# Performance work log

Measured on AMD Instinct MI355X. Metric: run time of the kernel, lower is better.

The kernel has to match this reference:

```python
import math
import jax, jax.numpy as jnp
import numpy as np

# dims (match init_kwargs)
B, NMHC, T, D = 4, 4, 1024, 256
DK, DATTN, H, E = 16, 512, 8, 4
DV = DATTN // H          # 64
DKP = 2 * DK             # 32 (PoPE doubles d_key)
HE = H * E
R = max(DK // 4, 1)      # 4
DA = int(DK * 1.618)     # 25
DPG = max(int(DATTN * 0.618), 1)  # 316
ND = NMHC * D
EPS = 1e-6
ROUTE_TEMP = 1.0

def _rms(x):
    return x * jax.lax.rsqrt(jnp.mean(x * x, axis=-1, keepdims=True) + EPS)

def _sinkhorn(M, n_iters=6):
    M = jnp.exp(M)
    for _ in range(n_iters):
        M = M / jnp.sum(M, axis=-1, keepdims=True)
        M = M / jnp.sum(M, axis=-2, keepdims=True)
    return M

def _l2norm(x):
    return x / jnp.maximum(jnp.linalg.norm(x, axis=-1, keepdims=True), 1e-12)

def _pope(x, phi):
    mu = jax.nn.softplus(x)
    return jnp.concatenate([mu * jnp.cos(phi), mu * jnp.sin(phi)], axis=-1)

def setup_inputs() -> dict:
    key = jax.random.key(0)
    ks = iter(jax.random.split(key, 40))
    rn = lambda shape, s=0.02: jax.random.normal(next(ks), shape, jnp.float32) * s
    return {
        'stream': jax.random.normal(next(ks), (B, NMHC, T, D), jnp.float32),
        'Wq': rn((H, D, DK)), 'Wk': rn((H, D, DK)), 'Wv': rn((H, D, DV)),
        'pope_delta': rn((DK,), 0.1),
        'q_router': rn((H, D, E), 0.05), 'kv_router': rn((H, D, E), 0.05),
        'lora_A_q': rn((HE, D, R), 0.01), 'lora_B_q': rn((HE, R, DK)),
        'lora_A_k': rn((HE, D, R), 0.01), 'lora_B_k': rn((HE, R, DK)),
        'lora_A_v': rn((HE, D, R), 0.01), 'lora_B_v': rn((HE, R, DV)),
        'alpha_up': rn((HE, D, DA), 0.01), 'alpha_down': rn((HE, DA, DKP), 0.01),
        'beta_up': rn((HE, D, DA), 0.01), 'beta_down': rn((HE, DA, 1), 0.01),
        'mhc_norm_w': jnp.ones((HE, ND)),
        'phi_pre': rn((HE, ND, NMHC)), 'phi_post': rn((HE, ND, NMHC)),
        'phi_res': rn((HE, ND, NMHC * NMHC)),
        'b_pre': jnp.zeros((HE, NMHC)), 'b_post': jnp.zeros((HE, NMHC)),
        'b_res': jnp.zeros((HE, NMHC, NMHC)),
        'a_pre': jnp.ones((HE,)), 'a_post': jnp.ones((HE,)), 'a_res': jnp.ones((HE,)),
        'norm_w': jnp.ones((HE, D)),
        'W_pre': rn((HE, D, DATTN), 0.01),
        'W_o': rn((DATTN, D)),
        'W_pg1': rn((HE, D, DPG), 0.01), 'W_pg2': rn((HE, DPG, D), 0.01),
    }

def _forward(stream, Wq, Wk, Wv, pope_delta, q_router, kv_router,
             lora_A_q, lora_B_q, lora_A_k, lora_B_k, lora_A_v, lora_B_v,
             alpha_up, alpha_down, beta_up, beta_down,
             mhc_norm_w, phi_pre, phi_post, phi_res, b_pre, b_post, b_res,
             a_pre, a_post, a_res, norm_w, W_pre, W_o, W_pg1, W_pg2):
    dt = stream.dtype
    freqs = 10000.0 ** (jnp.arange(DK, dtype=dt) / DK)
    pos = jnp.arange(T, dtype=dt)
    phi_q = pos[:, None] * freqs[None, :]                       # (T,DK)
    phi_k = phi_q - 2.0 * math.pi * jax.nn.sigmoid(pope_delta)  # key phase shift

    # MHC RMSNorm has no bias; fold its per-expert weight into the phi matrices
    x_hat = _rms(jnp.reshape(jnp.swapaxes(stream, 1, 2), (B, T, ND)))
    route_in = jnp.mean(stream, axis=1)                         # (B,T,D)

    q_logits = jnp.clip(jnp.einsum('btd,hde->hbte', route_in, q_router), -10, 10)
    q_probs = jax.nn.softmax(q_logits / ROUTE_TEMP, axis=-1)
    q_sel = jnp.argmax(q_logits, axis=-1)                       # (H,B,T) eval-mode routing
    kv_logits = jnp.clip(jnp.einsum('btd,hde->hbte', route_in, kv_router), -10, 10)
    kv_probs = jax.nn.softmax(kv_logits / ROUTE_TEMP, axis=-1)
    kv_sel = jnp.argmax(kv_logits, axis=-1)
    eidx = jnp.arange(E)

    acc_pre = jnp.zeros((B, T, H * DV), dt)
    acc_post = jnp.zeros((B, T, D), dt)
    acc_res = jnp.zeros((B, T, NMHC, NMHC), dt)
    acc_hpost = jnp.zeros((B, T, NMHC), dt)
    outs = []
    for h in range(H):
        s = slice(h * E, (h + 1) * E)
        nw = mhc_norm_w[s][:, :, None]
        Hpre = jax.nn.sigmoid(a_pre[s][:, None, None, None] * jnp.einsum('btk,ekn->ebtn', x_hat, nw * phi_pre[s]) + b_pre[s][:, None, None, :])
        Hpost = 2.0 * jax.nn.sigmoid(a_post[s][:, None, None, None] * jnp.einsum('btk,ekn->ebtn', x_hat, nw * phi_post[s]) + b_post[s][:, None, None, :])
        res_l = jnp.einsum('btk,ekm->ebtm', x_hat, nw * phi_res[s]).reshape(E, B, T, NMHC, NMHC)
        Hres = _sinkhorn(a_res[s][:, None, None, None, None] * res_l + b_res[s][:, None, None, :, :])

        he = jnp.einsum('ebtn,bntd->ebtd', Hpre, stream)        # (E,B,T,D)
        he = _rms(he) * norm_w[s][:, None, None, :]

        # straight-through routing weights (forward == hard mask)
        qp = jnp.moveaxis(q_probs[h], -1, 0)[..., None]         # (E,B,T,1)
        qm = (q_sel[h][None] == eidx[:, None, None]).astype(dt)[..., None]
        eff_q = qp + jax.lax.stop_gradient(qm - qp)
        kp = jnp.moveaxis(kv_probs[h], -1, 0)[..., None]
        km = (kv_sel[h][None] == eidx[:, None, None]).astype(dt)[..., None]
        eff_kv = kp + jax.lax.stop_gradient(km - kp)

        # Q path (expert 0 is a no-op for Q)
        dq = jnp.einsum('ebtr,erk->ebtk', jax.nn.silu(jnp.einsum('ebtd,edr->ebtr', he, lora_A_q[s])), lora_B_q[s])
        q_e = _pope(_l2norm(jnp.einsum('ebtd,dk->ebtk', he, Wq[h]) + dq), phi_q)
        pg = jax.nn.sigmoid(jnp.einsum('ebtp,epd->ebtd', jax.nn.silu(jnp.einsum('ebtd,edp->ebtp', he, W_pg1[s])), W_pg2[s]))
        q_h = jnp.sum(eff_q[1:] * q_e[1:], axis=0)
        acc_post = acc_post + jnp.sum(eff_q[1:] * pg[1:], axis=0) / H

        # KV path (all experts)
        dk_ = jnp.einsum('ebtr,erk->ebtk', jax.nn.silu(jnp.einsum('ebtd,edr->ebtr', he, lora_A_k[s])), lora_B_k[s])
        k_e = _pope(_l2norm(jnp.einsum('ebtd,dk->ebtk', he, Wk[h]) + dk_), phi_k)
        dv_ = jnp.einsum('ebtr,erk->ebtk', jax.nn.silu(jnp.einsum('ebtd,edr->ebtr', he, lora_A_v[s])), lora_B_v[s])
        v_e = jax.nn.silu(jnp.einsum('ebtd,dk->ebtk', he, Wv[h]) + dv_)
        al_e = jax.nn.sigmoid(jnp.einsum('ebta,eak->ebtk', jax.nn.silu(jnp.einsum('ebtd,eda->ebta', he, alpha_up[s])), alpha_down[s]))
        be_e = jax.nn.sigmoid(jnp.einsum('ebta,eak->ebtk', jax.nn.silu(jnp.einsum('ebtd,eda->ebta', he, beta_up[s])), beta_down[s]))
        preg = jax.nn.silu(jnp.einsum('ebtd,edc->ebtc', he, W_pre[s]))
        k_h = jnp.sum(eff_kv * k_e, axis=0)
        v_h = jnp.sum(eff_kv * v_e, axis=0)
        al_h = jnp.sum(eff_kv * al_e, axis=0)
        be_h = jnp.sum(eff_kv * be_e, axis=0)
        acc_pre = acc_pre + jnp.sum(eff_kv * preg, axis=0) / H
        acc_res = acc_res + jnp.sum(Hres * eff_kv[..., None], axis=0)
        acc_hpost = acc_hpost + jnp.sum(Hpost * eff_kv, axis=0)

        # KDA delta-rule recurrence over T (state S: (B,DKP,DV))
        def step(S, inp):
            q_t, k_t, v_t, a_t, b_t = inp
            aS = a_t[:, :, None] * S
            kaS = jnp.einsum('bd,bde->be', k_t, aS)
            S_new = aS + b_t[:, :, None] * (k_t[:, :, None] * (v_t - kaS)[:, None, :])
            return S_new, jnp.einsum('bd,bde->be', q_t, S_new)
        xs = tuple(jnp.swapaxes(a, 0, 1) for a in (q_h, k_h, v_h, al_h, be_h))
        _, o = jax.lax.scan(step, jnp.zeros((B, DKP, DV), dt), xs)
        out_h = jnp.where((q_sel[h] == 0)[..., None], jnp.zeros((), dt), jnp.swapaxes(o, 0, 1))
        outs.append(out_h)

    concat = jnp.concatenate(outs, axis=-1) / math.sqrt(H * DV)
    result = (concat * acc_pre) @ W_o * acc_post                # (B,T,D)
    res = jnp.einsum('btij,bjtd->bitd', acc_res / H, stream)    # stream mixing
    return res + jnp.einsum('btn,btd->bntd', acc_hpost / H, result)

def reference(stream, Wq, Wk, Wv, pope_delta, q_router, kv_router,
              lora_A_q, lora_B_q, lora_A_k, lora_B_k, lora_A_v, lora_B_v,
              alpha_up, alpha_down, beta_up, beta_down,
              mhc_norm_w, phi_pre, phi_post, phi_res, b_pre, b_post, b_res,
              a_pre, a_post, a_res, norm_w, W_pre, W_o, W_pg1, W_pg2):
    return _forward(stream, Wq, Wk, Wv, pope_delta, q_router, kv_router,
                    lora_A_q, lora_B_q, lora_A_k, lora_B_k, lora_A_v, lora_B_v,
                    alpha_up, alpha_down, beta_up, beta_down,
                    mhc_norm_w, phi_pre, phi_post, phi_res, b_pre, b_post, b_res,
                    a_pre, a_post, a_res, norm_w, W_pre, W_o, W_pg1, W_pg2)
```

## Files before the change

### kernel.cpp

```cpp
#include <hip/hip_runtime.h>
#include <math.h>

#define B_ 4
#define NM 4
#define T_ 1024
#define D_ 256
#define DK_ 16
#define DV_ 64
#define DKP_ 32
#define H_ 8
#define E_ 4
#define HE_ 32
#define R_ 4
#define DA_ 25
#define DPG_ 316
#define ND_ 1024
#define DATTN_ 512
#define BT_ 4096
#define TB 16
#define TT 64

#define OFF_CNT     0
#define OFF_ACCPRE  256
#define OFF_ACCPOST (OFF_ACCPRE + BT_*512)
#define OFF_ACCRES  (OFF_ACCPOST + BT_*256)
#define OFF_ACCHP   (OFF_ACCRES + BT_*16)
#define OFF_QH      (OFF_ACCHP + BT_*4)
#define ZERO_END    (OFF_QH + H_*BT_*32)
#define OFF_KH      ZERO_END
#define OFF_VH      (OFF_KH + H_*BT_*32)
#define OFF_ALH     (OFF_VH + H_*BT_*64)
#define OFF_BEH     (OFF_ALH + H_*BT_*32)
#define OFF_LKV     (OFF_BEH + H_*BT_)
#define OFF_LQ      (OFF_LKV + HE_*BT_)
#define OFF_RMS     (OFF_LQ + HE_*BT_)
#define OFF_ATTN    (OFF_RMS + BT_)
#define OFF_TRIG    (OFF_ATTN + BT_*512)
#define WS_FLOATS   (OFF_TRIG + 4*T_*DK_)

__device__ __forceinline__ float sigf(float x){ return 1.0f/(1.0f+expf(-x)); }
__device__ __forceinline__ float siluf(float x){ return x/(1.0f+expf(-x)); }
__device__ __forceinline__ float softplusf(float x){ return fmaxf(x,0.0f)+log1pf(expf(-fabsf(x))); }

__global__ __launch_bounds__(256) void k_trig(const float* __restrict__ delta, float* __restrict__ ws){
  int idx = blockIdx.x*256 + threadIdx.x;
  int t = idx >> 4, k = idx & 15;
  double fr = pow(10000.0, (double)k / 16.0);
  float freq = (float)fr;
  float pq = (float)t * freq;
  float sg = sigf(delta[k]);
  float shift = (float)(2.0*M_PI) * sg;
  float pk = pq - shift;
  float* tr = ws + OFF_TRIG;
  tr[idx]         = (float)cos((double)pq);
  tr[16384+idx]   = (float)sin((double)pq);
  tr[32768+idx]   = (float)cos((double)pk);
  tr[49152+idx]   = (float)sin((double)pk);
}

__global__ __launch_bounds__(256) void k_route(const float* __restrict__ stream,
    const float* __restrict__ q_router, const float* __restrict__ kv_router,
    float* __restrict__ ws){
  __shared__ float s_route[256];
  __shared__ float s_red[4];
  __shared__ float s_log[64];
  int tok = blockIdx.x; int b = tok >> 10, t = tok & 1023;
  int d = threadIdx.x;
  const float* sp = stream + ((size_t)(b*4)*1024 + t)*256 + d;
  float s0 = sp[0];
  float s1 = sp[1024*256];
  float s2 = sp[2*1024*256];
  float s3 = sp[3*1024*256];
  s_route[d] = (((s0+s1)+s2)+s3)*0.25f;
  float ssp = s0*s0+s1*s1+s2*s2+s3*s3;
  for (int off=32; off; off>>=1) ssp += __shfl_xor(ssp, off, 64);
  if ((d & 63)==0) s_red[d>>6] = ssp;
  __syncthreads();
  if (d==0){
    float ss = ((s_red[0]+s_red[1])+s_red[2])+s_red[3];
    float mean = ss*(1.0f/1024.0f) + 1e-6f;
    ws[OFF_RMS + tok] = (float)(1.0/sqrt((double)mean));
  }
  if (d < 64){
    int lane = d;
    int r = lane>>5, h = (lane>>2)&7, e = lane&3;
    const float* R = (r ? kv_router : q_router) + h*1024 + e;
    float acc = 0.f;
    for (int dd=0; dd<256; ++dd) acc = fmaf(s_route[dd], R[dd*4], acc);
    s_log[lane] = fminf(fmaxf(acc,-10.f),10.f);
  }
  if (d < 16){
    int r = d>>3, h = d&7;
    int base = r*32 + h*4;
    int best=0; float bv = s_log[base];
    for (int e=1;e<4;e++){ float v=s_log[base+e]; if (v>bv){bv=v;best=e;} }
    int* cnt = (int*)ws;
    if (r==1){
      int* lst = (int*)(ws + OFF_LKV);
      int pos = atomicAdd(&cnt[h*4+best],1);
      lst[(h*4+best)*BT_ + pos] = tok;
    } else if (best>0){
      int* lst = (int*)(ws + OFF_LQ);
      int pos = atomicAdd(&cnt[32 + h*4+best],1);
      lst[(h*4+best)*BT_ + pos] = tok;
    }
  }
}

__global__ __launch_bounds__(256) void k_expert_kv(
    const float* __restrict__ stream, float* ws,
    const float* __restrict__ Wk, const float* __restrict__ Wv,
    const float* __restrict__ lora_A_k, const float* __restrict__ lora_B_k,
    const float* __restrict__ lora_A_v, const float* __restrict__ lora_B_v,
    const float* __restrict__ alpha_up, const float* __restrict__ alpha_down,
    const float* __restrict__ beta_up, const float* __restrict__ beta_down,
    const float* __restrict__ mhc_norm_w, const float* __restrict__ phi_pre,
    const float* __restrict__ phi_post, const float* __restrict__ phi_res,
    const float* __restrict__ b_pre, const float* __restrict__ b_post, const float* __restrict__ b_res,
    const float* __restrict__ a_pre, const float* __restrict__ a_post, const float* __restrict__ a_res,
    const float* __restrict__ norm_w, const float* __restrict__ W_pre)
{
  int g = blockIdx.y; int h = g>>2;
  const int* cnt = (const int*)ws;
  int c = cnt[g];
  int start = blockIdx.x*TB;
  if (start >= c) return;
  int nact = min(TB, c-start);

  __shared__ float s_he[TB][258];
  __shared__ float s_phi[24][128];
  __shared__ float s_dots[TB][24];
  __shared__ float s_nw[1024];
  __shared__ float s_gnw[256];
  __shared__ float s_lrk[TB][4];
  __shared__ float s_lrv[TB][4];
  __shared__ float s_au[TB][25];
  __shared__ float s_bu[TB][25];
  __shared__ int s_tok[TB];
  int tid = threadIdx.x;
  if (tid < TB) s_tok[tid] = (tid < nact) ? ((const int*)(ws + OFF_LKV))[g*BT_ + start + tid] : -1;
  for (int i=tid;i<1024;i+=256) s_nw[i] = mhc_norm_w[g*1024+i];
  s_gnw[tid] = norm_w[g*256+tid];
  __syncthreads();

  float aP = a_pre[g], aQ = a_post[g], aR = a_res[g];
  int hw = tid>>5, lane = tid&31;
  int ti0 = hw, ti1 = hw+8;
  int tok0 = s_tok[ti0], tok1 = s_tok[ti1];
  const float* sb0 = stream + (tok0>=0 ? ((size_t)(tok0>>10)*4*262144 + (size_t)(tok0&1023)*256) : 0);
  const float* sb1 = stream + (tok1>=0 ? ((size_t)(tok1>>10)*4*262144 + (size_t)(tok1&1023)*256) : 0);
  float rn0 = (tok0>=0) ? ws[OFF_RMS + tok0] : 0.f;
  float rn1 = (tok1>=0) ? ws[OFF_RMS + tok1] : 0.f;

  float dA0[24], dA1[24];
  #pragma unroll
  for (int n=0;n<24;++n){ dA0[n]=0.f; dA1[n]=0.f; }
  for (int cc=0; cc<8; ++cc){
    __syncthreads();
    {
      int kk = tid & 127;
      int np = tid >> 7;
      int kg = cc*128 + kk;
      #pragma unroll
      for (int it=0; it<12; ++it){
        int n = np + it*2;
        float v;
        if (n < 4)       v = phi_pre [(size_t)g*4096  + (size_t)kg*4  + n];
        else if (n < 8)  v = phi_post[(size_t)g*4096  + (size_t)kg*4  + (n-4)];
        else             v = phi_res [(size_t)g*16384 + (size_t)kg*16 + (n-8)];
        s_phi[n][kk] = v;
      }
    }
    __syncthreads();
    int rr = cc>>1;
    int off = (cc&1)*128 + lane*4;
    float4 x0 = *(const float4*)(sb0 + (size_t)rr*262144 + off);
    float4 x1 = *(const float4*)(sb1 + (size_t)rr*262144 + off);
    float4 nw4 = *(const float4*)(&s_nw[cc*128 + lane*4]);
    x0.x *= rn0*nw4.x; x0.y *= rn0*nw4.y; x0.z *= rn0*nw4.z; x0.w *= rn0*nw4.w;
    x1.x *= rn1*nw4.x; x1.y *= rn1*nw4.y; x1.z *= rn1*nw4.z; x1.w *= rn1*nw4.w;
    #pragma unroll
    for (int n=0;n<24;++n){
      float4 p4 = *(const float4*)(&s_phi[n][lane*4]);
      dA0[n] = fmaf(x0.w,p4.w,fmaf(x0.z,p4.z,fmaf(x0.y,p4.y,fmaf(x0.x,p4.x,dA0[n]))));
      dA1[n] = fmaf(x1.w,p4.w,fmaf(x1.z,p4.z,fmaf(x1.y,p4.y,fmaf(x1.x,p4.x,dA1[n]))));
    }
  }
  #pragma unroll
  for (int n=0;n<24;++n){
    float v0=dA0[n], v1=dA1[n];
    v0 += __shfl_xor(v0,16,32); v0 += __shfl_xor(v0,8,32); v0 += __shfl_xor(v0,4,32); v0 += __shfl_xor(v0,2,32); v0 += __shfl_xor(v0,1,32);
    v1 += __shfl_xor(v1,16,32); v1 += __shfl_xor(v1,8,32); v1 += __shfl_xor(v1,4,32); v1 += __shfl_xor(v1,2,32); v1 += __shfl_xor(v1,1,32);
    dA0[n]=v0; dA1[n]=v1;
  }
  float bp0=b_pre[g*4+0], bp1=b_pre[g*4+1], bp2=b_pre[g*4+2], bp3=b_pre[g*4+3];

  auto finish = [&](int ti, int tok, const float (&dAx)[24], const float* sbx){
    if (tok < 0){
      #pragma unroll
      for (int m=0;m<8;++m) s_he[ti][m*32+lane] = 0.f;
      return;
    }
    if (lane==0){
      #pragma unroll
      for (int n=0;n<24;++n) s_dots[ti][n] = dAx[n];
    }
    float g0 = sigf(aP*dAx[0]+bp0);
    float g1 = sigf(aP*dAx[1]+bp1);
    float g2 = sigf(aP*dAx[2]+bp2);
    float g3 = sigf(aP*dAx[3]+bp3);
    if (lane>=16 && lane<20){
      int n = lane-16;
      float hp = 2.f*sigf(aQ*s_dots[ti][4+n] + b_post[g*4+n]);
      unsafeAtomicAdd(ws + OFF_ACCHP + tok*4 + n, hp);
    }
    if (lane<16){
      float m = expf(aR*s_dots[ti][8+lane] + b_res[g*16+lane]);
      for (int itr=0; itr<6; ++itr){
        float rsum = m;
        rsum += __shfl_xor(rsum, 1, 4);
        rsum += __shfl_xor(rsum, 2, 4);
        m = m / rsum;
        float csum = m;
        csum += __shfl_xor(csum, 4, 16);
        csum += __shfl_xor(csum, 8, 16);
        m = m / csum;
      }
      unsafeAtomicAdd(ws + OFF_ACCRES + tok*16 + lane, m);
    }
    float he[8]; float ssp = 0.f;
    #pragma unroll
    for (int m=0;m<8;++m){
      int d = m*32+lane;
      float hv = fmaf(g3, sbx[3*262144+d], fmaf(g2, sbx[2*262144+d], fmaf(g1, sbx[262144+d], g0*sbx[d])));
      he[m]=hv; ssp = fmaf(hv,hv,ssp);
    }
    ssp += __shfl_xor(ssp,16,32); ssp += __shfl_xor(ssp,8,32); ssp += __shfl_xor(ssp,4,32);
    ssp += __shfl_xor(ssp,2,32);  ssp += __shfl_xor(ssp,1,32);
    float scale = (float)(1.0/sqrt((double)(ssp*(1.0f/256.0f)+1e-6f)));
    #pragma unroll
    for (int m=0;m<8;++m){
      int d = m*32+lane;
      s_he[ti][d] = he[m]*scale*s_gnw[d];
    }
  };
  finish(ti0, tok0, dA0, sb0);
  finish(ti1, tok1, dA1, sb1);
  __syncthreads();

  if (tid < 128){
    int tt = (tid & 63) >> 2, r = tid & 3;
    const float* A = (tid < 64 ? lora_A_k : lora_A_v) + g*1024 + r;
    float acc = 0.f;
    for (int dd=0; dd<256; ++dd) acc = fmaf(s_he[tt][dd], A[dd*4], acc);
    float sv = siluf(acc);
    if (tid<64) s_lrk[tt][r] = sv; else s_lrv[tt][r] = sv;
  }
  __syncthreads();
  {
    int tt = tid>>4, kk = tid&15;
    float acc=0.f;
    const float* Wkp = Wk + h*4096 + kk;
    for (int dd=0; dd<256; ++dd) acc = fmaf(s_he[tt][dd], Wkp[dd*16], acc);
    float dkv = 0.f;
    for (int r=0;r<4;r++) dkv = fmaf(s_lrk[tt][r], lora_B_k[g*64 + r*16 + kk], dkv);
    acc += dkv;
    float ssq = acc*acc;
    ssq += __shfl_xor(ssq, 1, 16);
    ssq += __shfl_xor(ssq, 2, 16);
    ssq += __shfl_xor(ssq, 4, 16);
    ssq += __shfl_xor(ssq, 8, 16);
    float den = fmaxf(sqrtf(ssq), 1e-12f);
    float xn = acc/den;
    float mu = softplusf(xn);
    if (tt < nact){
      int tok = s_tok[tt]; int t = tok&1023;
      float* kh = ws + OFF_KH + ((size_t)h*BT_ + tok)*32;
      const float* ck = ws + OFF_TRIG + 32768;
      const float* sk = ws + OFF_TRIG + 49152;
      kh[kk]    = mu*ck[t*16+kk];
      kh[16+kk] = mu*sk[t*16+kk];
    }
  }
  for (int pass=0; pass<4; ++pass){
    int tt = pass*4 + (tid>>6), col = tid&63;
    float acc=0.f;
    const float* Wvp = Wv + h*16384 + col;
    for (int dd=0; dd<256; ++dd) acc = fmaf(s_he[tt][dd], Wvp[dd*64], acc);
    for (int r=0;r<4;r++) acc = fmaf(s_lrv[tt][r], lora_B_v[g*256 + r*64 + col], acc);
    if (tt < nact)
      ws[OFF_VH + ((size_t)h*BT_ + s_tok[tt])*64 + col] = siluf(acc);
  }
  for (int idx = tid; idx < nact*25; idx += 256){
    int tt = idx/25, aa = idx%25;
    const float* Au = alpha_up + g*6400 + aa;
    float acc=0.f;
    for (int dd=0; dd<256; ++dd) acc = fmaf(s_he[tt][dd], Au[dd*25], acc);
    s_au[tt][aa] = siluf(acc);
    const float* Bu = beta_up + g*6400 + aa;
    float acc2=0.f;
    for (int dd=0; dd<256; ++dd) acc2 = fmaf(s_he[tt][dd], Bu[dd*25], acc2);
    s_bu[tt][aa] = siluf(acc2);
  }
  __syncthreads();
  for (int idx = tid; idx < nact*32; idx += 256){
    int tt = idx>>5, kk = idx&31;
    float acc=0.f;
    for (int aa=0; aa<25; ++aa) acc = fmaf(s_au[tt][aa], alpha_down[g*800 + aa*32 + kk], acc);
    ws[OFF_ALH + ((size_t)h*BT_ + s_tok[tt])*32 + kk] = sigf(acc);
  }
  if (tid < nact){
    float acc=0.f;
    for (int aa=0; aa<25; ++aa) acc = fmaf(s_bu[tid][aa], beta_down[g*25+aa], acc);
    ws[OFF_BEH + (size_t)h*BT_ + s_tok[tid]] = sigf(acc);
  }
  {
    float acc0[TB], acc1[TB];
    #pragma unroll
    for (int tt=0;tt<TB;++tt){acc0[tt]=0.f;acc1[tt]=0.f;}
    const float* Wp = W_pre + (size_t)g*131072;
    for (int dd=0; dd<256; ++dd){
      float w0 = Wp[dd*512 + tid];
      float w1 = Wp[dd*512 + 256 + tid];
      #pragma unroll
      for (int tt=0;tt<TB;++tt){
        float hvv = s_he[tt][dd];
        acc0[tt] = fmaf(hvv, w0, acc0[tt]);
        acc1[tt] = fmaf(hvv, w1, acc1[tt]);
      }
    }
    for (int tt=0;tt<nact;++tt){
      int tok = s_tok[tt];
      unsafeAtomicAdd(ws + OFF_ACCPRE + (size_t)tok*512 + tid,       siluf(acc0[tt]));
      unsafeAtomicAdd(ws + OFF_ACCPRE + (size_t)tok*512 + 256 + tid, siluf(acc1[tt]));
    }
  }
}

__global__ __launch_bounds__(256) void k_expert_q(
    const float* __restrict__ stream, float* ws,
    const float* __restrict__ Wq, const float* __restrict__ lora_A_q, const float* __restrict__ lora_B_q,
    const float* __restrict__ mhc_norm_w, const float* __restrict__ phi_pre,
    const float* __restrict__ b_pre, const float* __restrict__ a_pre,
    const float* __restrict__ norm_w, const float* __restrict__ W_pg1, const float* __restrict__ W_pg2)
{
  int g = blockIdx.y; int h = g>>2;
  const int* cnt = (const int*)ws;
  int c = cnt[32+g];
  int start = blockIdx.x*TB;
  if (start >= c) return;
  int nact = min(TB, c-start);

  __shared__ float s_he[TB][258];
  __shared__ float s_u[TB][DPG_];
  __shared__ float s_nw[1024];
  __shared__ float s_gnw[256];
  __shared__ float s_lrq[TB][4];
  __shared__ int s_tok[TB];
  int tid = threadIdx.x;
  if (tid < TB) s_tok[tid] = (tid<nact) ? ((const int*)(ws + OFF_LQ))[g*BT_ + start + tid] : -1;
  for (int i=tid;i<1024;i+=256) s_nw[i] = mhc_norm_w[g*1024+i];
  s_gnw[tid] = norm_w[g*256+tid];
  __syncthreads();
  float aP = a_pre[g];
  int hw = tid>>5, lane = tid&31;

  for (int ii=0; ii<2; ++ii){
    int ti = hw + ii*8;
    int tok = s_tok[ti];
    if (tok < 0){
      #pragma unroll
      for (int m=0;m<8;++m) s_he[ti][m*32+lane] = 0.f;
      continue;
    }
    int b = tok>>10, t = tok&1023;
    const float* sb = stream + ((size_t)b*4*1024 + (size_t)t)*256;
    float rms = ws[OFF_RMS + tok];
    const float4* ppre = (const float4*)(phi_pre + (size_t)g*4096);
    float d0=0.f,d1=0.f,d2=0.f,d3=0.f;
    #pragma unroll 4
    for (int j=0;j<32;++j){
      int k = j*32 + lane;
      float xv = sb[(size_t)(k>>8)*262144 + (k&255)] * rms * s_nw[k];
      float4 pa = ppre[k];
      d0=fmaf(xv,pa.x,d0); d1=fmaf(xv,pa.y,d1); d2=fmaf(xv,pa.z,d2); d3=fmaf(xv,pa.w,d3);
    }
    d0 += __shfl_xor(d0,16,32); d0 += __shfl_xor(d0,8,32); d0 += __shfl_xor(d0,4,32); d0 += __shfl_xor(d0,2,32); d0 += __shfl_xor(d0,1,32);
    d1 += __shfl_xor(d1,16,32); d1 += __shfl_xor(d1,8,32); d1 += __shfl_xor(d1,4,32); d1 += __shfl_xor(d1,2,32); d1 += __shfl_xor(d1,1,32);
    d2 += __shfl_xor(d2,16,32); d2 += __shfl_xor(d2,8,32); d2 += __shfl_xor(d2,4,32); d2 += __shfl_xor(d2,2,32); d2 += __shfl_xor(d2,1,32);
    d3 += __shfl_xor(d3,16,32); d3 += __shfl_xor(d3,8,32); d3 += __shfl_xor(d3,4,32); d3 += __shfl_xor(d3,2,32); d3 += __shfl_xor(d3,1,32);
    float g0 = sigf(aP*d0+b_pre[g*4+0]);
    float g1 = sigf(aP*d1+b_pre[g*4+1]);
    float g2 = sigf(aP*d2+b_pre[g*4+2]);
    float g3 = sigf(aP*d3+b_pre[g*4+3]);
    float he[8]; float ssp = 0.f;
    #pragma unroll
    for (int m=0;m<8;++m){
      int d = m*32+lane;
      float hv = fmaf(g3, sb[3*262144+d], fmaf(g2, sb[2*262144+d], fmaf(g1, sb[262144+d], g0*sb[d])));
      he[m]=hv; ssp = fmaf(hv,hv,ssp);
    }
    ssp += __shfl_xor(ssp,16,32); ssp += __shfl_xor(ssp,8,32); ssp += __shfl_xor(ssp,4,32);
    ssp += __shfl_xor(ssp,2,32);  ssp += __shfl_xor(ssp,1,32);
    float scale = (float)(1.0/sqrt((double)(ssp*(1.0f/256.0f)+1e-6f)));
    #pragma unroll
    for (int m=0;m<8;++m){
      int d = m*32+lane;
      s_he[ti][d] = he[m]*scale*s_gnw[d];
    }
  }
  __syncthreads();

  if (tid<64){
    int tt=tid>>2, r=tid&3;
    const float* A = lora_A_q + g*1024 + r;
    float acc=0.f;
    for (int dd=0;dd<256;++dd) acc = fmaf(s_he[tt][dd], A[dd*4], acc);
    s_lrq[tt][r] = siluf(acc);
  }
  __syncthreads();
  {
    int tt=tid>>4, kk=tid&15;
    const float* Wqp = Wq + h*4096 + kk;
    float acc=0.f;
    for (int dd=0;dd<256;++dd) acc = fmaf(s_he[tt][dd], Wqp[dd*16], acc);
    float dq=0.f;
    for (int r=0;r<4;r++) dq = fmaf(s_lrq[tt][r], lora_B_q[g*64+r*16+kk], dq);
    acc += dq;
    float ssq = acc*acc;
    ssq += __shfl_xor(ssq,1,16); ssq += __shfl_xor(ssq,2,16);
    ssq += __shfl_xor(ssq,4,16); ssq += __shfl_xor(ssq,8,16);
    float den = fmaxf(sqrtf(ssq),1e-12f);
    float xn = acc/den;
    float mu = softplusf(xn);
    if (tt<nact){
      int tok=s_tok[tt]; int t=tok&1023;
      float* qh = ws + OFF_QH + ((size_t)h*BT_+tok)*32;
      const float* cq = ws + OFF_TRIG;
      const float* sq = ws + OFF_TRIG + 16384;
      qh[kk]    = mu*cq[t*16+kk];
      qh[16+kk] = mu*sq[t*16+kk];
    }
  }
  {
    float accq[TB], accq2[TB];
    #pragma unroll
    for (int tt=0;tt<TB;++tt){ accq[tt]=0.f; accq2[tt]=0.f; }
    int p = tid;
    int p2 = 256 + tid;
    bool has2 = (p2 < DPG_);
    const float* Wp  = W_pg1 + (size_t)g*80896 + p;
    const float* Wp2 = W_pg1 + (size_t)g*80896 + (has2 ? p2 : p);
    for (int dd=0;dd<256;++dd){
      float w  = Wp [(size_t)dd*316];
      float w2 = Wp2[(size_t)dd*316];
      #pragma unroll
      for (int tt=0;tt<TB;++tt){
        float hvv = s_he[tt][dd];
        accq[tt]  = fmaf(hvv, w,  accq[tt]);
        accq2[tt] = fmaf(hvv, w2, accq2[tt]);
      }
    }
    #pragma unroll
    for (int tt=0;tt<TB;++tt){
      s_u[tt][p] = siluf(accq[tt]);
      if (has2) s_u[tt][p2] = siluf(accq2[tt]);
    }
  }
  __syncthreads();
  {
    float acc2[TB];
    #pragma unroll
    for (int tt=0;tt<TB;++tt) acc2[tt]=0.f;
    const float* Wp2 = W_pg2 + (size_t)g*80896 + tid;
    for (int p=0;p<DPG_;++p){
      float w = Wp2[(size_t)p*256];
      #pragma unroll
      for (int tt=0;tt<TB;++tt) acc2[tt] = fmaf(s_u[tt][p], w, acc2[tt]);
    }
    for (int tt=0;tt<nact;++tt)
      unsafeAtomicAdd(ws + OFF_ACCPOST + (size_t)s_tok[tt]*256 + tid, sigf(acc2[tt]));
  }
}

__global__ __launch_bounds__(256) void k_kda(float* ws){
  int hb = blockIdx.x; int h = hb>>2, b = hb&3;
  int tid = threadIdx.x;
  int e = tid >> 2, dg = tid & 3;
  const float* qb = ws + OFF_QH  + ((size_t)h*BT_ + b*T_)*32;
  const float* kb = ws + OFF_KH  + ((size_t)h*BT_ + b*T_)*32;
  const float* ab = ws + OFF_ALH + ((size_t)h*BT_ + b*T_)*32;
  const float* vb = ws + OFF_VH  + ((size_t)h*BT_ + b*T_)*64;
  const float* bb = ws + OFF_BEH + (size_t)h*BT_ + b*T_;
  float* ob = ws + OFF_ATTN + (size_t)b*T_*512 + h*64;

  __shared__ float s_q[TT*32];
  __shared__ float s_k[TT*32];
  __shared__ float s_a[TT*32];
  __shared__ float s_v[TT*64];
  __shared__ float s_b[TT];
  __shared__ float s_o[TT*64];

  float S[8];
  #pragma unroll
  for (int j=0;j<8;++j) S[j]=0.f;

  for (int t0=0; t0<T_; t0+=TT){
    {
      const float4* q4 = (const float4*)(qb + t0*32);
      const float4* k4 = (const float4*)(kb + t0*32);
      const float4* a4 = (const float4*)(ab + t0*32);
      const float4* v4 = (const float4*)(vb + t0*64);
      #pragma unroll
      for (int r=0;r<2;++r){
        int i = r*256 + tid;
        ((float4*)s_q)[i] = q4[i];
        ((float4*)s_k)[i] = k4[i];
        ((float4*)s_a)[i] = a4[i];
      }
      #pragma unroll
      for (int r=0;r<4;++r){
        int i = r*256 + tid;
        ((float4*)s_v)[i] = v4[i];
      }
      if (tid < TT) s_b[tid] = bb[t0+tid];
    }
    __syncthreads();
    #pragma unroll 4
    for (int tt=0; tt<TT; ++tt){
      const float* kp = s_k + tt*32 + dg*8;
      const float* ap = s_a + tt*32 + dg*8;
      const float* qp = s_q + tt*32 + dg*8;
      float v  = s_v[tt*64 + e];
      float be = s_b[tt];
      float part = 0.f;
      float kv[8], av[8];
      #pragma unroll
      for (int j=0;j<8;++j){ kv[j]=kp[j]; av[j]=ap[j]; part = fmaf(kv[j]*av[j], S[j], part); }
      part += __shfl_xor(part, 1, 4);
      part += __shfl_xor(part, 2, 4);
      float w = be*(v - part);
      float op = 0.f;
      #pragma unroll
      for (int j=0;j<8;++j){
        S[j] = fmaf(w, kv[j], av[j]*S[j]);
        op = fmaf(qp[j], S[j], op);
      }
      op += __shfl_xor(op, 1, 4);
      op += __shfl_xor(op, 2, 4);
      if (dg==0) s_o[tt*64 + e] = op / 22.627416997969522f;
    }
    __syncthreads();
    for (int i=tid; i<TT*16; i+=256){
      int tt = i>>4, c = i&15;
      ((float4*)(ob + (size_t)(t0+tt)*512))[c] = ((const float4*)(s_o + tt*64))[c];
    }
  }
}

__global__ __launch_bounds__(256) void k_final(const float* __restrict__ stream,
    const float* __restrict__ W_o, float* ws, float* __restrict__ out){
  __shared__ float s_m[8][512];
  __shared__ float s_rs[8][16];
  __shared__ float s_hp[8][4];
  int tid = threadIdx.x;
  int t0 = blockIdx.x*8;
  for (int tt=0;tt<8;++tt){
    int tok = t0+tt;
    for (int idx=tid; idx<512; idx+=256)
      s_m[tt][idx] = ws[OFF_ATTN + (size_t)tok*512 + idx] * (0.125f*ws[OFF_ACCPRE + (size_t)tok*512 + idx]);
    if (tid<16) s_rs[tt][tid] = 0.125f*ws[OFF_ACCRES + tok*16 + tid];
    if (tid<4)  s_hp[tt][tid] = 0.125f*ws[OFF_ACCHP + tok*4 + tid];
  }
  __syncthreads();
  float facc[8];
  #pragma unroll
  for (int tt=0;tt<8;++tt) facc[tt]=0.f;
  const float* Wop = W_o + tid;
  for (int cc=0;cc<512;++cc){
    float w = Wop[(size_t)cc*256];
    #pragma unroll
    for (int tt=0;tt<8;++tt) facc[tt] = fmaf(s_m[tt][cc], w, facc[tt]);
  }
  for (int tt=0;tt<8;++tt){
    int tok=t0+tt; int b=tok>>10, t=tok&1023;
    float result = facc[tt]*(0.125f*ws[OFF_ACCPOST + (size_t)tok*256 + tid]);
    float st[4];
    #pragma unroll
    for (int j=0;j<4;++j) st[j]=stream[(((size_t)b*4+j)*1024+t)*256+tid];
    #pragma unroll
    for (int n=0;n<4;++n){
      float rv = fmaf(s_rs[tt][n*4+3], st[3],
                 fmaf(s_rs[tt][n*4+2], st[2],
                 fmaf(s_rs[tt][n*4+1], st[1], s_rs[tt][n*4]*st[0])));
      out[(((size_t)b*4+n)*1024+t)*256+tid] = rv + s_hp[tt][n]*result;
    }
  }
}

extern "C" void kernel_launch(void* const* d_in, const int* in_sizes, int n_in,
                              void* d_out, int out_size, void* d_ws, size_t ws_size,
                              hipStream_t stream){
  const float* s = (const float*)d_in[0];
  float* ws = (float*)d_ws;
  hipMemsetAsync(d_ws, 0, (size_t)ZERO_END*4, stream);
  k_trig<<<64,256,0,stream>>>((const float*)d_in[4], ws);
  k_route<<<4096,256,0,stream>>>(s, (const float*)d_in[5], (const float*)d_in[6], ws);
  dim3 g2(BT_/TB, 32);
  k_expert_kv<<<g2,256,0,stream>>>(s, ws,
      (const float*)d_in[2],  (const float*)d_in[3],
      (const float*)d_in[9],  (const float*)d_in[10],
      (const float*)d_in[11], (const float*)d_in[12],
      (const float*)d_in[13], (const float*)d_in[14],
      (const float*)d_in[15], (const float*)d_in[16],
      (const float*)d_in[17], (const float*)d_in[18],
      (const float*)d_in[19], (const float*)d_in[20],
      (const float*)d_in[21], (const float*)d_in[22], (const float*)d_in[23],
      (const float*)d_in[24], (const float*)d_in[25], (const float*)d_in[26],
      (const float*)d_in[27], (const float*)d_in[28]);
  k_expert_q<<<g2,256,0,stream>>>(s, ws,
      (const float*)d_in[1],  (const float*)d_in[7], (const float*)d_in[8],
      (const float*)d_in[17], (const float*)d_in[18],
      (const float*)d_in[21], (const float*)d_in[24],
      (const float*)d_in[27], (const float*)d_in[30], (const float*)d_in[31]);
  k_kda<<<32,256,0,stream>>>(ws);
  k_final<<<512,256,0,stream>>>(s, (const float*)d_in[29], ws, (float*)d_out);
}
```

Measured before the change: 1.509 ms.

## Double expert token tile to 32 with 512-thread blocks

Raises the per-block token tile in both expert kernels from 16 to 32 and launches 512 threads per block, remapping the thread-to-work assignments (phi staging, LoRA, value and W_pre projections, and the W_pg1/W_pg2 gating passes). Each weight element loaded from global memory is now reused across twice as many tokens, which cuts weight traffic per token. The cost is larger shared-memory footprints and more per-thread accumulators (up to 32 registers in W_pre and W_pg1), which may lower occupancy. Some index mappings, such as the K projection block using tid>>4, may not have been fully adapted to the new tile.

```diff
diff --git a/kernel.cpp b/kernel.cpp
--- a/kernel.cpp
+++ b/kernel.cpp
@@ -17,7 +17,7 @@
 #define ND_ 1024
 #define DATTN_ 512
 #define BT_ 4096
-#define TB 16
+#define TB 32
 #define TT 64
 
 #define OFF_CNT     0
@@ -107,7 +107,7 @@
   }
 }
 
-__global__ __launch_bounds__(256) void k_expert_kv(
+__global__ __launch_bounds__(512,4) void k_expert_kv(
     const float* __restrict__ stream, float* ws,
     const float* __restrict__ Wk, const float* __restrict__ Wv,
     const float* __restrict__ lora_A_k, const float* __restrict__ lora_B_k,
@@ -139,13 +139,13 @@
   __shared__ int s_tok[TB];
   int tid = threadIdx.x;
   if (tid < TB) s_tok[tid] = (tid < nact) ? ((const int*)(ws + OFF_LKV))[g*BT_ + start + tid] : -1;
-  for (int i=tid;i<1024;i+=256) s_nw[i] = mhc_norm_w[g*1024+i];
-  s_gnw[tid] = norm_w[g*256+tid];
+  for (int i=tid;i<1024;i+=512) s_nw[i] = mhc_norm_w[g*1024+i];
+  if (tid < 256) s_gnw[tid] = norm_w[g*256+tid];
   __syncthreads();
 
   float aP = a_pre[g], aQ = a_post[g], aR = a_res[g];
   int hw = tid>>5, lane = tid&31;
-  int ti0 = hw, ti1 = hw+8;
+  int ti0 = hw, ti1 = hw+16;
   int tok0 = s_tok[ti0], tok1 = s_tok[ti1];
   const float* sb0 = stream + (tok0>=0 ? ((size_t)(tok0>>10)*4*262144 + (size_t)(tok0&1023)*256) : 0);
   const float* sb1 = stream + (tok1>=0 ? ((size_t)(tok1>>10)*4*262144 + (size_t)(tok1&1023)*256) : 0);
@@ -162,8 +162,8 @@
       int np = tid >> 7;
       int kg = cc*128 + kk;
       #pragma unroll
-      for (int it=0; it<12; ++it){
-        int n = np + it*2;
+      for (int it=0; it<6; ++it){
+        int n = np + it*4;
         float v;
         if (n < 4)       v = phi_pre [(size_t)g*4096  + (size_t)kg*4  + n];
         else if (n < 8)  v = phi_post[(size_t)g*4096  + (size_t)kg*4  + (n-4)];
@@ -248,13 +248,13 @@
   finish(ti1, tok1, dA1, sb1);
   __syncthreads();
 
-  if (tid < 128){
-    int tt = (tid & 63) >> 2, r = tid & 3;
-    const float* A = (tid < 64 ? lora_A_k : lora_A_v) + g*1024 + r;
+  if (tid < 256){
+    int tt = (tid & 127) >> 2, r = tid & 3;
+    const float* A = (tid < 128 ? lora_A_k : lora_A_v) + g*1024 + r;
     float acc = 0.f;
     for (int dd=0; dd<256; ++dd) acc = fmaf(s_he[tt][dd], A[dd*4], acc);
     float sv = siluf(acc);
-    if (tid<64) s_lrk[tt][r] = sv; else s_lrv[tt][r] = sv;
+    if (tid<128) s_lrk[tt][r] = sv; else s_lrv[tt][r] = sv;
   }
   __syncthreads();
   {
@@ -283,7 +283,7 @@
     }
   }
   for (int pass=0; pass<4; ++pass){
-    int tt = pass*4 + (tid>>6), col = tid&63;
+    int tt = pass*8 + (tid>>6), col = tid&63;
     float acc=0.f;
     const float* Wvp = Wv + h*16384 + col;
     for (int dd=0; dd<256; ++dd) acc = fmaf(s_he[tt][dd], Wvp[dd*64], acc);
@@ -291,7 +291,7 @@
     if (tt < nact)
       ws[OFF_VH + ((size_t)h*BT_ + s_tok[tt])*64 + col] = siluf(acc);
   }
-  for (int idx = tid; idx < nact*25; idx += 256){
+  for (int idx = tid; idx < nact*25; idx += 512){
     int tt = idx/25, aa = idx%25;
     const float* Au = alpha_up + g*6400 + aa;
     float acc=0.f;
@@ -303,7 +303,7 @@
     s_bu[tt][aa] = siluf(acc2);
   }
   __syncthreads();
-  for (int idx = tid; idx < nact*32; idx += 256){
+  for (int idx = tid; idx < nact*32; idx += 512){
     int tt = idx>>5, kk = idx&31;
     float acc=0.f;
     for (int aa=0; aa<25; ++aa) acc = fmaf(s_au[tt][aa], alpha_down[g*800 + aa*32 + kk], acc);
@@ -315,29 +315,21 @@
     ws[OFF_BEH + (size_t)h*BT_ + s_tok[tid]] = sigf(acc);
   }
   {
-    float acc0[TB], acc1[TB];
-    #pragma unroll
-    for (int tt=0;tt<TB;++tt){acc0[tt]=0.f;acc1[tt]=0.f;}
-    const float* Wp = W_pre + (size_t)g*131072;
+    float acc[TB];
+    #pragma unroll
+    for (int tt=0;tt<TB;++tt) acc[tt]=0.f;
+    const float* Wp = W_pre + (size_t)g*131072 + tid;
     for (int dd=0; dd<256; ++dd){
-      float w0 = Wp[dd*512 + tid];
-      float w1 = Wp[dd*512 + 256 + tid];
-      #pragma unroll
-      for (int tt=0;tt<TB;++tt){
-        float hvv = s_he[tt][dd];
-        acc0[tt] = fmaf(hvv, w0, acc0[tt]);
-        acc1[tt] = fmaf(hvv, w1, acc1[tt]);
-      }
-    }
-    for (int tt=0;tt<nact;++tt){
-      int tok = s_tok[tt];
-      unsafeAtomicAdd(ws + OFF_ACCPRE + (size_t)tok*512 + tid,       siluf(acc0[tt]));
-      unsafeAtomicAdd(ws + OFF_ACCPRE + (size_t)tok*512 + 256 + tid, siluf(acc1[tt]));
-    }
+      float w = Wp[(size_t)dd*512];
+      #pragma unroll
+      for (int tt=0;tt<TB;++tt) acc[tt] = fmaf(s_he[tt][dd], w, acc[tt]);
+    }
+    for (int tt=0;tt<nact;++tt)
+      unsafeAtomicAdd(ws + OFF_ACCPRE + (size_t)s_tok[tt]*512 + tid, siluf(acc[tt]));
   }
 }
 
-__global__ __launch_bounds__(256) void k_expert_q(
+__global__ __launch_bounds__(512,4) void k_expert_q(
     const float* __restrict__ stream, float* ws,
     const float* __restrict__ Wq, const float* __restrict__ lora_A_q, const float* __restrict__ lora_B_q,
     const float* __restrict__ mhc_norm_w, const float* __restrict__ phi_pre,
@@ -359,14 +351,14 @@
   __shared__ int s_tok[TB];
   int tid = threadIdx.x;
   if (tid < TB) s_tok[tid] = (tid<nact) ? ((const int*)(ws + OFF_LQ))[g*BT_ + start + tid] : -1;
-  for (int i=tid;i<1024;i+=256) s_nw[i] = mhc_norm_w[g*1024+i];
-  s_gnw[tid] = norm_w[g*256+tid];
+  for (int i=tid;i<1024;i+=512) s_nw[i] = mhc_norm_w[g*1024+i];
+  if (tid < 256) s_gnw[tid] = norm_w[g*256+tid];
   __syncthreads();
   float aP = a_pre[g];
   int hw = tid>>5, lane = tid&31;
 
   for (int ii=0; ii<2; ++ii){
-    int ti = hw + ii*8;
+    int ti = hw + ii*16;
     int tok = s_tok[ti];
     if (tok < 0){
       #pragma unroll
@@ -411,7 +403,7 @@
   }
   __syncthreads();
 
-  if (tid<64){
+  if (tid<128){
     int tt=tid>>2, r=tid&3;
     const float* A = lora_A_q + g*1024 + r;
     float acc=0.f;
@@ -442,44 +434,37 @@
       qh[16+kk] = mu*sq[t*16+kk];
     }
   }
+  if (tid < DPG_){
+    float acc[TB];
+    #pragma unroll
+    for (int tt=0;tt<TB;++tt) acc[tt]=0.f;
+    const float* Wp = W_pg1 + (size_t)g*80896 + tid;
+    for (int dd=0;dd<256;++dd){
+      float w = Wp[(size_t)dd*316];
+      #pragma unroll
+      for (int tt=0;tt<TB;++tt) acc[tt] = fmaf(s_he[tt][dd], w, acc[tt]);
+    }
+    #pragma unroll
+    for (int tt=0;tt<TB;++tt) s_u[tt][tid] = siluf(acc[tt]);
+  }
+  __syncthreads();
   {
-    float accq[TB], accq2[TB];
-    #pragma unroll
-    for (int tt=0;tt<TB;++tt){ accq[tt]=0.f; accq2[tt]=0.f; }
-    int p = tid;
-    int p2 = 256 + tid;
-    bool has2 = (p2 < DPG_);
-    const float* Wp  = W_pg1 + (size_t)g*80896 + p;
-    const float* Wp2 = W_pg1 + (size_t)g*80896 + (has2 ? p2 : p);
-    for (int dd=0;dd<256;++dd){
-      float w  = Wp [(size_t)dd*316];
-      float w2 = Wp2[(size_t)dd*316];
-      #pragma unroll
-      for (int tt=0;tt<TB;++tt){
-        float hvv = s_he[tt][dd];
-        accq[tt]  = fmaf(hvv, w,  accq[tt]);
-        accq2[tt] = fmaf(hvv, w2, accq2[tt]);
-      }
-    }
-    #pragma unroll
-    for (int tt=0;tt<TB;++tt){
-      s_u[tt][p] = siluf(accq[tt]);
-      if (has2) s_u[tt][p2] = siluf(accq2[tt]);
-    }
-  }
-  __syncthreads();
-  {
-    float acc2[TB];
-    #pragma unroll
-    for (int tt=0;tt<TB;++tt) acc2[tt]=0.f;
-    const float* Wp2 = W_pg2 + (size_t)g*80896 + tid;
+    int half = tid>>8, col = tid&255;
+    float acc2[16];
+    #pragma unroll
+    for (int j=0;j<16;++j) acc2[j]=0.f;
+    const float* Wp2 = W_pg2 + (size_t)g*80896 + col;
     for (int p=0;p<DPG_;++p){
       float w = Wp2[(size_t)p*256];
       #pragma unroll
-      for (int tt=0;tt<TB;++tt) acc2[tt] = fmaf(s_u[tt][p], w, acc2[tt]);
-    }
-    for (int tt=0;tt<nact;++tt)
-      unsafeAtomicAdd(ws + OFF_ACCPOST + (size_t)s_tok[tt]*256 + tid, sigf(acc2[tt]));
+      for (int j=0;j<16;++j) acc2[j] = fmaf(s_u[half*16+j][p], w, acc2[j]);
+    }
+    #pragma unroll
+    for (int j=0;j<16;++j){
+      int tt = half*16 + j;
+      if (tt < nact)
+        unsafeAtomicAdd(ws + OFF_ACCPOST + (size_t)s_tok[tt]*256 + col, sigf(acc2[j]));
+    }
   }
 }
 
@@ -607,7 +592,7 @@
   k_trig<<<64,256,0,stream>>>((const float*)d_in[4], ws);
   k_route<<<4096,256,0,stream>>>(s, (const float*)d_in[5], (const float*)d_in[6], ws);
   dim3 g2(BT_/TB, 32);
-  k_expert_kv<<<g2,256,0,stream>>>(s, ws,
+  k_expert_kv<<<g2,512,0,stream>>>(s, ws,
       (const float*)d_in[2],  (const float*)d_in[3],
       (const float*)d_in[9],  (const float*)d_in[10],
       (const float*)d_in[11], (const float*)d_in[12],
@@ -618,7 +603,7 @@
       (const float*)d_in[21], (const float*)d_in[22], (const float*)d_in[23],
       (const float*)d_in[24], (const float*)d_in[25], (const float*)d_in[26],
       (const float*)d_in[27], (const float*)d_in[28]);
-  k_expert_q<<<g2,256,0,stream>>>(s, ws,
+  k_expert_q<<<g2,512,0,stream>>>(s, ws,
       (const float*)d_in[1],  (const float*)d_in[7], (const float*)d_in[8],
       (const float*)d_in[17], (const float*)d_in[18],
       (const float*)d_in[21], (const float*)d_in[24],
```

Result: slower. 1.674 ms (+10.9%).
